# Performance work log

Measured on AMD Instinct MI355X. Metric: run time of the kernel, lower is better.

The kernel has to match this reference:

```python
import jax, jax.numpy as jnp
import numpy as np

N_NODES = 50000


def gcn_layer(x, src, dst, ew, W, b, n_nodes):
    # PyG GCNConv: add self-loops (weight 1), symmetric deg^-1/2 normalization,
    # linear transform, scatter-add aggregation at destination, then bias.
    loop = jnp.arange(n_nodes, dtype=src.dtype)
    s = jnp.concatenate([src, loop])
    d = jnp.concatenate([dst, loop])
    w = jnp.concatenate([ew, jnp.ones((n_nodes,), dtype=ew.dtype)])
    deg = jax.ops.segment_sum(w, d, num_segments=n_nodes)  # [N]
    dinv = jnp.where(deg > 0, jax.lax.rsqrt(jnp.where(deg > 0, deg, 1.0)), 0.0)
    norm = dinv[s] * w * dinv[d]  # [E+N]
    h = x @ W  # [N, out]
    msg = h[s] * norm[:, None]  # gather + scale, [E+N, out]
    out = jax.ops.segment_sum(msg, d, num_segments=n_nodes)  # scatter-add
    return out + b


def setup_inputs() -> dict:
    key = jax.random.key(0)
    k1, k2, k3, k4, k5, k6, k7 = jax.random.split(key, 7)
    N, E, C_IN, C_OUT = N_NODES, 600000, 128, 128
    x = jax.random.normal(k1, (N, C_IN), dtype=jnp.float32)
    edge_index = jax.random.randint(k2, (2, E), 0, N, dtype=jnp.int64)
    edge_weight = jax.random.uniform(k3, (E,), dtype=jnp.float32)
    # Glorot-style init like PyG's Linear default
    s1 = 1.0 / np.sqrt(C_IN)
    s2 = 1.0 / np.sqrt(C_OUT)
    W1 = jax.random.uniform(k4, (C_IN, C_OUT), jnp.float32, -s1, s1)
    b1 = jnp.zeros((C_OUT,), dtype=jnp.float32)
    W2 = jax.random.uniform(k5, (C_OUT, C_OUT), jnp.float32, -s2, s2)
    b2 = jnp.zeros((C_OUT,), dtype=jnp.float32)
    return {"x": x, "edge_index": edge_index, "edge_weight": edge_weight,
            "W1": W1, "b1": b1, "W2": W2, "b2": b2}


def reference(x, edge_index, edge_weight, W1, b1, W2, b2):
    src, dst = edge_index[0], edge_index[1]
    h = jax.nn.relu(gcn_layer(x, src, dst, edge_weight, W1, b1, N_NODES))
    return jax.nn.relu(gcn_layer(h, src, dst, edge_weight, W2, b2, N_NODES))
```

## Files before the change

kernel.cpp:

```cpp
#include <hip/hip_runtime.h>
#include <math.h>

#define CH   128
#define CH4  32
#define TPB  256
#define SCANB 1024
#define WIMG 16384
#define NREP 4
#define FIXS 1048576.0f

typedef __attribute__((ext_vector_type(8))) short short8;
typedef __attribute__((ext_vector_type(4))) float floatx4;
typedef __attribute__((ext_vector_type(8))) float float8;
typedef unsigned long long u64;

static __device__ __forceinline__ unsigned short f2bf(float f) {
    unsigned u = __float_as_uint(f);
    return (unsigned short)((u + 0x7fffu + ((u >> 16) & 1u)) >> 16);
}
static __device__ __forceinline__ float bf2f(unsigned short s) {
    return __uint_as_float(((unsigned)s) << 16);
}
static __device__ __forceinline__ float8 bf8_to_f8(short8 u) {
    float8 f;
    #pragma unroll
    for (int i = 0; i < 8; ++i) f[i] = bf2f((unsigned short)u[i]);
    return f;
}

__global__ void k_prep(const float* __restrict__ W1, const float* __restrict__ W2,
                       short* __restrict__ Wsplit, float4* __restrict__ zbase,
                       int nzero4, int nbPrep) {
    int bx = blockIdx.x;
    if (bx >= nbPrep) {
        int i = (bx - nbPrep) * TPB + threadIdx.x;
        if (i < nzero4) zbase[i] = make_float4(0.f, 0.f, 0.f, 0.f);
        return;
    }
    int i = bx * TPB + threadIdx.x;
    if (i >= 2 * CH * CH) return;
    int layer = i >> 14;
    int idx   = i & 16383;
    int k = idx >> 7, c = idx & 127;
    float w = (layer ? W2 : W1)[k * CH + c];
    unsigned short hi = f2bf(w);
    unsigned short lo = f2bf(w - bf2f(hi));
    int colh = c >> 6, nn = c & 63;
    int kt = k >> 5, q = (k & 31) >> 3, j = k & 7;
    int ns = nn >> 4, ln = q * 16 + (nn & 15);
    size_t base = (size_t)(layer * 2 + colh) * WIMG;
    size_t off  = ((size_t)(kt * 4 + ns) * 64 + ln) * 8 + j;
    Wsplit[base + off]        = (short)hi;
    Wsplit[base + 8192 + off] = (short)lo;
}

static __device__ __forceinline__ void gemm_body_f32(
        const float* __restrict__ X, const short* __restrict__ Wfrag,
        unsigned short* __restrict__ H, int n, int tile, int colh, int tid) {
    __shared__ __align__(16) short sW[2][4][4][64][8];
    {
        const float4* gsrc = (const float4*)Wfrag;
        float4* ldst = (float4*)sW;
        #pragma unroll
        for (int i = 0; i < 8; ++i)
            ldst[i * TPB + tid] = gsrc[i * TPB + tid];
    }
    __syncthreads();

    const int lane = tid & 63;
    const int wv   = tid >> 6;
    const int q    = lane >> 4;
    const int m    = lane & 15;
    const int row0 = tile * 64 + wv * 16;
    if (row0 >= n) return;

    int rrow = row0 + m;
    if (rrow > n - 1) rrow = n - 1;

    const float4* xr = (const float4*)(X + (size_t)rrow * CH);
    float4 xa[4][2];
    #pragma unroll
    for (int kt = 0; kt < 4; ++kt) {
        xa[kt][0] = xr[kt * 8 + q * 2 + 0];
        xa[kt][1] = xr[kt * 8 + q * 2 + 1];
    }

    floatx4 acc[4];
    #pragma unroll
    for (int ns = 0; ns < 4; ++ns) acc[ns] = (floatx4){0.f, 0.f, 0.f, 0.f};

    #pragma unroll
    for (int kt = 0; kt < 4; ++kt) {
        float xf[8] = { xa[kt][0].x, xa[kt][0].y, xa[kt][0].z, xa[kt][0].w,
                        xa[kt][1].x, xa[kt][1].y, xa[kt][1].z, xa[kt][1].w };
        short8 ah, al;
        #pragma unroll
        for (int j = 0; j < 8; ++j) {
            float v = xf[j];
            unsigned short h = f2bf(v);
            ah[j] = (short)h;
            al[j] = (short)f2bf(v - bf2f(h));
        }
        #pragma unroll
        for (int ns = 0; ns < 4; ++ns) {
            short8 bh = *(const short8*)&sW[0][kt][ns][lane][0];
            short8 bl = *(const short8*)&sW[1][kt][ns][lane][0];
            acc[ns] = __builtin_amdgcn_mfma_f32_16x16x32_bf16(ah, bh, acc[ns], 0, 0, 0);
            acc[ns] = __builtin_amdgcn_mfma_f32_16x16x32_bf16(al, bh, acc[ns], 0, 0, 0);
            acc[ns] = __builtin_amdgcn_mfma_f32_16x16x32_bf16(ah, bl, acc[ns], 0, 0, 0);
        }
    }

    #pragma unroll
    for (int ns = 0; ns < 4; ++ns) {
        #pragma unroll
        for (int reg = 0; reg < 4; ++reg) {
            int r = row0 + q * 4 + reg;
            if (r < n)
                H[(size_t)r * CH + colh * 64 + ns * 16 + m] = f2bf(acc[ns][reg]);
        }
    }
}

__global__ __launch_bounds__(TPB, 4)
void k_gemm_rank(const float* __restrict__ X, const short* __restrict__ Wsplit,
                 unsigned short* __restrict__ H, int n,
                 const int* __restrict__ dst, const float* __restrict__ ew,
                 u64* __restrict__ counts_rep, int* __restrict__ rank,
                 int E, int nbE4, int Np) {
    int bx = blockIdx.x;
    if (bx < nbE4) {
        int stride = nbE4 * TPB;
        int e = bx * TPB + threadIdx.x;
        #pragma unroll
        for (int it = 0; it < 4; ++it, e += stride) {
            if (e < E) {
                int d = dst[e];
                if ((unsigned)d < (unsigned)n) {
                    int rep = e & (NREP - 1);
                    u64 pk = (1ull << 40) |
                             (u64)(unsigned)__float2uint_rn(ew[e] * FIXS);
                    u64 old = atomicAdd(&counts_rep[(size_t)rep * Np + d], pk);
                    rank[e] = (int)(old >> 40);
                }
            }
        }
    } else {
        bx -= nbE4;
        int colh = bx & 1;
        gemm_body_f32(X, Wsplit + (size_t)colh * WIMG, H, n, bx >> 1, colh,
                      threadIdx.x);
    }
}

__global__ __launch_bounds__(SCANB)
void k_scan1(const u64* __restrict__ counts_rep, int Np,
             int* __restrict__ counts_tot, int* __restrict__ repoff,
             int* __restrict__ row_start, float* __restrict__ dinv,
             int* __restrict__ partials, int* __restrict__ pp_s,
             int* __restrict__ done, int nb, int n) {
    __shared__ int swt[SCANB / 64];
    __shared__ int slastS;
    const int tid  = threadIdx.x;
    const int lane = tid & 63;
    const int wid  = tid >> 6;
    const int gid  = blockIdx.x * SCANB + tid;

    int c[NREP];
    int v = 0;
    u64 wsum = 0;
    #pragma unroll
    for (int r = 0; r < NREP; ++r) {
        u64 pk = (gid < n) ? counts_rep[(size_t)r * Np + gid] : 0ull;
        c[r] = (int)(pk >> 40);
        wsum += pk & ((1ull << 40) - 1);
        v += c[r];
    }
    int inc = v;
    #pragma unroll
    for (int off = 1; off < 64; off <<= 1) {
        int t = __shfl_up(inc, off, 64);
        if (lane >= off) inc += t;
    }
    if (lane == 63) swt[wid] = inc;
    __syncthreads();
    if (wid == 0) {
        int wv_ = (lane < SCANB / 64) ? swt[lane] : 0;
        int winc = wv_;
        #pragma unroll
        for (int off = 1; off < SCANB / 64; off <<= 1) {
            int t = __shfl_up(winc, off, 64);
            if (lane >= off) winc += t;
        }
        if (lane < SCANB / 64) swt[lane] = winc - wv_;
    }
    __syncthreads();
    const int myincl = inc + swt[wid];

    if (gid < n) {
        row_start[gid]  = myincl - v;
        counts_tot[gid] = v;
        dinv[gid] = rsqrtf(1.0f + (float)wsum * (1.0f / FIXS));
        int pre = 0;
        int ro[NREP];
        #pragma unroll
        for (int r = 0; r < NREP; ++r) { ro[r] = pre; pre += c[r]; }
        ((int4*)repoff)[gid] = make_int4(ro[0], ro[1], ro[2], ro[3]);
    }
    if (tid == SCANB - 1) {
        partials[blockIdx.x] = myincl;
        __threadfence();
        int old = atomicAdd(done, 1);
        slastS = (old == nb - 1);
    }
    __syncthreads();
    if (slastS && tid < 64) {
        int pv = (tid < nb) ? atomicAdd(&partials[tid], 0) : 0;
        int i2 = pv;
        #pragma unroll
        for (int off = 1; off < 64; off <<= 1) {
            int t = __shfl_up(i2, off, 64);
            if ((tid & 63) >= off) i2 += t;
        }
        if (tid < nb) pp_s[tid] = i2 - pv;
    }
}

__global__ void k_fill(const int* __restrict__ src, const int* __restrict__ dst,
                       const float* __restrict__ ew, const int* __restrict__ row_start,
                       const int* __restrict__ pp_s, const int* __restrict__ repoff,
                       const int* __restrict__ rank, const float* __restrict__ dinv,
                       int2* __restrict__ edges, int E, int n) {
    int e = blockIdx.x * blockDim.x + threadIdx.x;
    if (e >= E) return;
    int s = src[e], d = dst[e];
    if ((unsigned)s >= (unsigned)n || (unsigned)d >= (unsigned)n) return;
    int rep = e & (NREP - 1);
    int base = row_start[d] + pp_s[d >> 10] + repoff[d * NREP + rep];
    edges[base + rank[e]] = make_int2(s, __float_as_int(ew[e] * dinv[s]));
}

static __device__ __forceinline__ float8 agg_node8(
        const short8* __restrict__ h8, const int2* __restrict__ edges,
        float di, const float8 b, int node, int tx,
        const int* __restrict__ row_start, const int* __restrict__ pp_s,
        const int* __restrict__ counts) {
    float8 hv = bf8_to_f8(h8[(size_t)node * 16 + tx]);
    float8 acc;
    #pragma unroll
    for (int i = 0; i < 8; ++i) acc[i] = 0.f;

    int j   = row_start[node] + pp_s[node >> 10];
    int end = j + counts[node];

    int2 e[8];
    bool have = (j + 8 <= end);
    if (have) {
        #pragma unroll
        for (int i = 0; i < 8; ++i) e[i] = edges[j + i];
    }
    while (have) {
        short8 g[8];
        #pragma unroll
        for (int i = 0; i < 8; ++i) g[i] = h8[(size_t)e[i].x * 16 + tx];
        int2 en[8];
        const bool haven = (j + 16 <= end);
        if (haven) {
            #pragma unroll
            for (int i = 0; i < 8; ++i) en[i] = edges[j + 8 + i];
        }
        #pragma unroll
        for (int i = 0; i < 8; ++i) {
            float w = __int_as_float(e[i].y);
            float8 gf = bf8_to_f8(g[i]);
            #pragma unroll
            for (int c = 0; c < 8; ++c) acc[c] += gf[c] * w;
        }
        j += 8;
        have = haven;
        #pragma unroll
        for (int i = 0; i < 8; ++i) e[i] = en[i];
    }
    if (j + 4 <= end) {
        int2 e4[4];
        #pragma unroll
        for (int i = 0; i < 4; ++i) e4[i] = edges[j + i];
        short8 g[4];
        #pragma unroll
        for (int i = 0; i < 4; ++i) g[i] = h8[(size_t)e4[i].x * 16 + tx];
        #pragma unroll
        for (int i = 0; i < 4; ++i) {
            float w = __int_as_float(e4[i].y);
            float8 gf = bf8_to_f8(g[i]);
            #pragma unroll
            for (int c = 0; c < 8; ++c) acc[c] += gf[c] * w;
        }
        j += 4;
    }
    for (; j < end; ++j) {
        int2 e0 = edges[j];
        float w0 = __int_as_float(e0.y);
        float8 gf = bf8_to_f8(h8[(size_t)e0.x * 16 + tx]);
        #pragma unroll
        for (int c = 0; c < 8; ++c) acc[c] += gf[c] * w0;
    }

    float di2 = di * di;
    float8 o;
    #pragma unroll
    for (int c = 0; c < 8; ++c) o[c] = di2 * hv[c] + di * acc[c] + b[c];
    return o;
}

__global__ __launch_bounds__(TPB)
void k_agg_gemm(const unsigned short* __restrict__ h,
                const int* __restrict__ row_start, const int* __restrict__ pp_s,
                const int* __restrict__ counts, const int2* __restrict__ edges,
                const float* __restrict__ dinv, const float* __restrict__ bias,
                const short* __restrict__ W2img,
                unsigned short* __restrict__ h2, int n) {
    __shared__ __align__(16) short8 tile[16 * 17];
    const int tid = threadIdx.x;

    const int bnode0 = (int)blockIdx.x * 16;
    const int tx = tid & 15;
    const int tg = tid >> 4;
    const int node = bnode0 + tg;
    float8 b;
    #pragma unroll
    for (int c = 0; c < 8; ++c) b[c] = bias[tx * 8 + c];
    short8 u;
    if (node < n) {
        float8 o = agg_node8((const short8*)h, edges, dinv[node], b, node,
                             tx, row_start, pp_s, counts);
        #pragma unroll
        for (int c = 0; c < 8; ++c) u[c] = (short)f2bf(fmaxf(o[c], 0.f));
    } else {
        #pragma unroll
        for (int c = 0; c < 8; ++c) u[c] = 0;
    }
    tile[tg * 17 + tx] = u;
    __syncthreads();

    const int lane = tid & 63;
    const int wv   = tid >> 6;
    const int q    = lane >> 4;
    const int m    = lane & 15;
    const int ch   = wv & 1;
    const int ns0  = (wv >> 1) * 2;

    short8 a[4];
    #pragma unroll
    for (int kt = 0; kt < 4; ++kt)
        a[kt] = tile[m * 17 + kt * 4 + q];

    const short8* w2f = (const short8*)(W2img + (size_t)ch * WIMG);

    floatx4 acc[2];
    #pragma unroll
    for (int i = 0; i < 2; ++i) acc[i] = (floatx4){0.f, 0.f, 0.f, 0.f};

    #pragma unroll
    for (int kt = 0; kt < 4; ++kt) {
        #pragma unroll
        for (int i = 0; i < 2; ++i) {
            short8 bh = w2f[(kt * 4 + ns0 + i) * 64 + lane];
            acc[i] = __builtin_amdgcn_mfma_f32_16x16x32_bf16(a[kt], bh, acc[i],
                                                             0, 0, 0);
        }
    }

    #pragma unroll
    for (int i = 0; i < 2; ++i)
        #pragma unroll
        for (int reg = 0; reg < 4; ++reg) {
            int r = bnode0 + q * 4 + reg;
            if (r < n)
                h2[(size_t)r * CH + ch * 64 + (ns0 + i) * 16 + m] =
                    f2bf(acc[i][reg]);
        }
}

__global__ __launch_bounds__(TPB)
void k_aggregate2(const unsigned short* __restrict__ h,
                  const int* __restrict__ row_start, const int* __restrict__ pp_s,
                  const int* __restrict__ counts, const int2* __restrict__ edges,
                  const float* __restrict__ dinv, const float* __restrict__ bias,
                  float* __restrict__ out, int n) {
    int t = blockIdx.x * blockDim.x + threadIdx.x;
    int node = t >> 4;
    if (node >= n) return;
    int tx = t & 15;
    float8 b;
    #pragma unroll
    for (int c = 0; c < 8; ++c) b[c] = bias[tx * 8 + c];
    float8 o = agg_node8((const short8*)h, edges, dinv[node], b, node, tx,
                         row_start, pp_s, counts);
    float4 lo = make_float4(fmaxf(o[0], 0.f), fmaxf(o[1], 0.f),
                            fmaxf(o[2], 0.f), fmaxf(o[3], 0.f));
    float4 hi = make_float4(fmaxf(o[4], 0.f), fmaxf(o[5], 0.f),
                            fmaxf(o[6], 0.f), fmaxf(o[7], 0.f));
    ((float4*)out)[(size_t)node * CH4 + tx * 2 + 0] = lo;
    ((float4*)out)[(size_t)node * CH4 + tx * 2 + 1] = hi;
}

extern "C" void kernel_launch(void* const* d_in, const int* in_sizes, int n_in,
                              void* d_out, int out_size, void* d_ws, size_t ws_size,
                              hipStream_t stream) {
    const float* x  = (const float*)d_in[0];
    const int*   ei = (const int*)d_in[1];
    const float* ew = (const float*)d_in[2];
    const float* W1 = (const float*)d_in[3];
    const float* b1 = (const float*)d_in[4];
    const float* W2 = (const float*)d_in[5];
    const float* b2 = (const float*)d_in[6];
    float* out = (float*)d_out;

    const int N = in_sizes[0] / CH;
    const int E = in_sizes[2];
    const int* src = ei;
    const int* dst = ei + E;

    size_t Np = ((size_t)N + 255) & ~(size_t)255;
    size_t Ep = ((size_t)E + 63) & ~(size_t)63;
    float* ws          = (float*)d_ws;
    float* dinv        = ws;
    unsigned short* h  = (unsigned short*)(dinv + Np);
    unsigned short* h2 = h + (size_t)N * CH;
    u64*   counts_rep  = (u64*)(h2 + (size_t)N * CH);
    int*   done        = (int*)(counts_rep + NREP * Np);
    int    nzero4      = (int)((2 * NREP * Np + 64) / 4);
    int*  counts_tot   = done + 64;
    int*  row_start    = counts_tot + Np;
    int*  repoff       = row_start + Np;
    int*  rank         = repoff + NREP * Np;
    int*  partials     = rank + Ep;
    int*  pp_s         = partials + 64;
    int2* edges        = (int2*)(pp_s + 64);
    short* Wsplit      = (short*)(edges + E);

    const int nbE    = (E + TPB - 1) / TPB;
    const int nbE4   = (E + TPB * 4 - 1) / (TPB * 4);
    const int nbAgg  = (int)(((size_t)N * 16 + TPB - 1) / TPB);
    const int nbScan = (N + SCANB - 1) / SCANB;
    const int nbGemm = 2 * ((N + 63) / 64);
    const int nbAG   = (N + 15) / 16;
    const int nbPrep = (2 * CH * CH + TPB - 1) / TPB;
    const int nbZero = (nzero4 + TPB - 1) / TPB;

    k_prep     <<<nbPrep + nbZero, TPB, 0, stream>>>(W1, W2, Wsplit,
                                                     (float4*)counts_rep,
                                                     nzero4, nbPrep);

    k_gemm_rank<<<nbE4 + nbGemm, TPB, 0, stream>>>(x, Wsplit, h, N, dst, ew,
                                                   counts_rep, rank, E, nbE4,
                                                   (int)Np);
    k_scan1    <<<nbScan, SCANB, 0, stream>>>(counts_rep, (int)Np, counts_tot,
                                              repoff, row_start, dinv,
                                              partials, pp_s, done, nbScan, N);
    k_fill     <<<nbE, TPB, 0, stream>>>(src, dst, ew, row_start, pp_s, repoff,
                                         rank, dinv, edges, E, N);

    k_agg_gemm <<<nbAG, TPB, 0, stream>>>(h, row_start, pp_s, counts_tot,
                                          edges, dinv, b1,
                                          Wsplit + 2 * (size_t)WIMG, h2, N);
    k_aggregate2<<<nbAgg, TPB, 0, stream>>>(h2, row_start, pp_s, counts_tot,
                                            edges, dinv, b2, out, N);
}
```

Before: 210.1 us.

## Derive CSR slots by atomic decrement in fill; drop rank array, use 8 replicas

The counting pass now uses fire-and-forget atomic adds and no longer stores a per-edge rank. The fill kernel instead claims a slot by atomically decrementing the replica counter and taking the returned count. The number of counter replicas goes from 4 to 8 to reduce atomic contention, and the aggregation loop drops its software-prefetch double-buffering of edge records. This removes the rank array's writes and reads, but adds a returning atomic to the fill kernel and doubles the counter memory that has to be zeroed and scanned.

```diff
diff --git a/kernel.cpp b/kernel.cpp
--- a/kernel.cpp
+++ b/kernel.cpp
@@ -6,7 +6,7 @@
 #define TPB  256
 #define SCANB 1024
 #define WIMG 16384
-#define NREP 4
+#define NREP 8
 #define FIXS 1048576.0f
 
 typedef __attribute__((ext_vector_type(8))) short short8;
@@ -126,8 +126,7 @@
 void k_gemm_rank(const float* __restrict__ X, const short* __restrict__ Wsplit,
                  unsigned short* __restrict__ H, int n,
                  const int* __restrict__ dst, const float* __restrict__ ew,
-                 u64* __restrict__ counts_rep, int* __restrict__ rank,
-                 int E, int nbE4, int Np) {
+                 u64* __restrict__ counts_rep, int E, int nbE4, int Np) {
     int bx = blockIdx.x;
     if (bx < nbE4) {
         int stride = nbE4 * TPB;
@@ -140,8 +139,7 @@
                     int rep = e & (NREP - 1);
                     u64 pk = (1ull << 40) |
                              (u64)(unsigned)__float2uint_rn(ew[e] * FIXS);
-                    u64 old = atomicAdd(&counts_rep[(size_t)rep * Np + d], pk);
-                    rank[e] = (int)(old >> 40);
+                    atomicAdd(&counts_rep[(size_t)rep * Np + d], pk);
                 }
             }
         }
@@ -155,7 +153,7 @@
 
 __global__ __launch_bounds__(SCANB)
 void k_scan1(const u64* __restrict__ counts_rep, int Np,
-             int* __restrict__ counts_tot, int* __restrict__ repoff,
+             int* __restrict__ counts_tot, int* __restrict__ repoff8,
              int* __restrict__ row_start, float* __restrict__ dinv,
              int* __restrict__ partials, int* __restrict__ pp_s,
              int* __restrict__ done, int nb, int n) {
@@ -205,7 +203,8 @@
         int ro[NREP];
         #pragma unroll
         for (int r = 0; r < NREP; ++r) { ro[r] = pre; pre += c[r]; }
-        ((int4*)repoff)[gid] = make_int4(ro[0], ro[1], ro[2], ro[3]);
+        ((int4*)repoff8)[gid * 2 + 0] = make_int4(ro[0], ro[1], ro[2], ro[3]);
+        ((int4*)repoff8)[gid * 2 + 1] = make_int4(ro[4], ro[5], ro[6], ro[7]);
     }
     if (tid == SCANB - 1) {
         partials[blockIdx.x] = myincl;
@@ -228,16 +227,18 @@
 
 __global__ void k_fill(const int* __restrict__ src, const int* __restrict__ dst,
                        const float* __restrict__ ew, const int* __restrict__ row_start,
-                       const int* __restrict__ pp_s, const int* __restrict__ repoff,
-                       const int* __restrict__ rank, const float* __restrict__ dinv,
-                       int2* __restrict__ edges, int E, int n) {
+                       const int* __restrict__ pp_s, const int* __restrict__ repoff8,
+                       u64* __restrict__ counts_rep, const float* __restrict__ dinv,
+                       int2* __restrict__ edges, int E, int n, int Np) {
     int e = blockIdx.x * blockDim.x + threadIdx.x;
     if (e >= E) return;
     int s = src[e], d = dst[e];
     if ((unsigned)s >= (unsigned)n || (unsigned)d >= (unsigned)n) return;
     int rep = e & (NREP - 1);
-    int base = row_start[d] + pp_s[d >> 10] + repoff[d * NREP + rep];
-    edges[base + rank[e]] = make_int2(s, __float_as_int(ew[e] * dinv[s]));
+    u64 old = atomicAdd(&counts_rep[(size_t)rep * Np + d], 0ull - (1ull << 40));
+    int slot = (int)(old >> 40) - 1;
+    int base = row_start[d] + pp_s[d >> 10] + repoff8[d * NREP + rep];
+    edges[base + slot] = make_int2(s, __float_as_int(ew[e] * dinv[s]));
 }
 
 static __device__ __forceinline__ float8 agg_node8(
@@ -253,22 +254,13 @@
     int j   = row_start[node] + pp_s[node >> 10];
     int end = j + counts[node];
 
-    int2 e[8];
-    bool have = (j + 8 <= end);
-    if (have) {
+    for (; j + 8 <= end; j += 8) {
+        int2 e[8];
         #pragma unroll
         for (int i = 0; i < 8; ++i) e[i] = edges[j + i];
-    }
-    while (have) {
         short8 g[8];
         #pragma unroll
         for (int i = 0; i < 8; ++i) g[i] = h8[(size_t)e[i].x * 16 + tx];
-        int2 en[8];
-        const bool haven = (j + 16 <= end);
-        if (haven) {
-            #pragma unroll
-            for (int i = 0; i < 8; ++i) en[i] = edges[j + 8 + i];
-        }
         #pragma unroll
         for (int i = 0; i < 8; ++i) {
             float w = __int_as_float(e[i].y);
@@ -276,21 +268,17 @@
             #pragma unroll
             for (int c = 0; c < 8; ++c) acc[c] += gf[c] * w;
         }
-        j += 8;
-        have = haven;
-        #pragma unroll
-        for (int i = 0; i < 8; ++i) e[i] = en[i];
     }
     if (j + 4 <= end) {
-        int2 e4[4];
-        #pragma unroll
-        for (int i = 0; i < 4; ++i) e4[i] = edges[j + i];
+        int2 e[4];
+        #pragma unroll
+        for (int i = 0; i < 4; ++i) e[i] = edges[j + i];
         short8 g[4];
         #pragma unroll
-        for (int i = 0; i < 4; ++i) g[i] = h8[(size_t)e4[i].x * 16 + tx];
+        for (int i = 0; i < 4; ++i) g[i] = h8[(size_t)e[i].x * 16 + tx];
         #pragma unroll
         for (int i = 0; i < 4; ++i) {
-            float w = __int_as_float(e4[i].y);
+            float w = __int_as_float(e[i].y);
             float8 gf = bf8_to_f8(g[i]);
             #pragma unroll
             for (int c = 0; c < 8; ++c) acc[c] += gf[c] * w;
@@ -422,7 +410,6 @@
     const int* dst = ei + E;
 
     size_t Np = ((size_t)N + 255) & ~(size_t)255;
-    size_t Ep = ((size_t)E + 63) & ~(size_t)63;
     float* ws          = (float*)d_ws;
     float* dinv        = ws;
     unsigned short* h  = (unsigned short*)(dinv + Np);
@@ -432,9 +419,8 @@
     int    nzero4      = (int)((2 * NREP * Np + 64) / 4);
     int*  counts_tot   = done + 64;
     int*  row_start    = counts_tot + Np;
-    int*  repoff       = row_start + Np;
-    int*  rank         = repoff + NREP * Np;
-    int*  partials     = rank + Ep;
+    int*  repoff8      = row_start + Np;
+    int*  partials     = repoff8 + NREP * Np;
     int*  pp_s         = partials + 64;
     int2* edges        = (int2*)(pp_s + 64);
     short* Wsplit      = (short*)(edges + E);
@@ -453,13 +439,12 @@
                                                      nzero4, nbPrep);
 
     k_gemm_rank<<<nbE4 + nbGemm, TPB, 0, stream>>>(x, Wsplit, h, N, dst, ew,
-                                                   counts_rep, rank, E, nbE4,
-                                                   (int)Np);
+                                                   counts_rep, E, nbE4, (int)Np);
     k_scan1    <<<nbScan, SCANB, 0, stream>>>(counts_rep, (int)Np, counts_tot,
-                                              repoff, row_start, dinv,
+                                              repoff8, row_start, dinv,
                                               partials, pp_s, done, nbScan, N);
-    k_fill     <<<nbE, TPB, 0, stream>>>(src, dst, ew, row_start, pp_s, repoff,
-                                         rank, dinv, edges, E, N);
+    k_fill     <<<nbE, TPB, 0, stream>>>(src, dst, ew, row_start, pp_s, repoff8,
+                                         counts_rep, dinv, edges, E, N, (int)Np);
 
     k_agg_gemm <<<nbAG, TPB, 0, stream>>>(h, row_start, pp_s, counts_tot,
                                           edges, dinv, b1,
```

Result: slower. 223.7 us (+6.5%).
